# Kernel optimization log

Hardware: AMD Instinct MI355X
Metric: run time of the kernel (lower is better)

The kernel has to match this reference:

```python
import jax, jax.numpy as jnp
import numpy as np


def conv1x1(x, w, b):
    # x: [B,C,H,W], w: [O,C], b: [O]  (1x1 conv == per-pixel matmul)
    return jnp.einsum('oc,bchw->bohw', w, x) + b[None, :, None, None]


def setup_inputs() -> dict:
    key = jax.random.key(0)
    ks = jax.random.split(key, 8)
    B, C, H, W = 8, 256, 64, 64
    heads, points = 8, 4
    x = jax.random.normal(ks[0], (B, C, H, W), dtype=jnp.float32)
    # small offset weights so sampling grids stay mostly in-range (original inits these to 0)
    w_off = jax.random.normal(ks[1], (heads * points * 2, C), dtype=jnp.float32) * 0.01
    b_off = jax.random.normal(ks[2], (heads * points * 2,), dtype=jnp.float32) * 0.05
    w_attn = jax.random.normal(ks[3], (heads * points, C), dtype=jnp.float32) * 0.02
    b_attn = jnp.full((heads * points,), np.log(1.0 / points), dtype=jnp.float32)
    w_val = jax.random.normal(ks[4], (C, C), dtype=jnp.float32) * (1.0 / np.sqrt(C))
    b_val = jnp.zeros((C,), dtype=jnp.float32)
    w_out = jax.random.normal(ks[5], (C, C), dtype=jnp.float32) * (1.0 / np.sqrt(C))
    b_out = jnp.zeros((C,), dtype=jnp.float32)
    return {"x": x, "w_off": w_off, "b_off": b_off, "w_attn": w_attn, "b_attn": b_attn,
            "w_val": w_val, "b_val": b_val, "w_out": w_out, "b_out": b_out,
            "num_heads": heads, "num_points": points}


def _grid_sample_one(v, g):
    # v: [Cph,H,W] value image; g: [P,H,W,2] sampling grid in [-1,1] (x,y), align_corners=True,
    # bilinear, zero padding. Returns [Cph,P,H,W].
    Cph, H, W = v.shape
    ix = (g[..., 0] + 1.0) * 0.5 * (W - 1)  # [P,H,W]
    iy = (g[..., 1] + 1.0) * 0.5 * (H - 1)
    x0 = jnp.floor(ix); y0 = jnp.floor(iy)
    x1 = x0 + 1.0;      y1 = y0 + 1.0
    wx1 = ix - x0; wx0 = 1.0 - wx1
    wy1 = iy - y0; wy0 = 1.0 - wy1

    def corner(yc, xc, w):
        valid = (xc >= 0) & (xc <= W - 1) & (yc >= 0) & (yc <= H - 1)
        yi = jnp.clip(yc, 0, H - 1).astype(jnp.int32)
        xi = jnp.clip(xc, 0, W - 1).astype(jnp.int32)
        vv = v[:, yi, xi]  # [Cph,P,H,W]
        return vv * (w * valid.astype(w.dtype))[None]

    return (corner(y0, x0, wy0 * wx0) + corner(y0, x1, wy0 * wx1)
            + corner(y1, x0, wy1 * wx0) + corner(y1, x1, wy1 * wx1))


def deformable_attention(x, w_off, b_off, w_attn, b_attn, w_val, b_val, w_out, b_out,
                         num_heads, num_points):
    B, C, H, W = x.shape
    hd, P = num_heads, num_points
    cph = C // hd

    value = conv1x1(x, w_val, b_val)                       # [B,C,H,W]
    offsets = conv1x1(x, w_off, b_off)                     # [B,hd*P*2,H,W]
    attn = conv1x1(x, w_attn, b_attn).reshape(B, hd, P, H, W)
    attn = jax.nn.softmax(attn, axis=2)                    # softmax over points

    gy = jnp.linspace(-1.0, 1.0, H, dtype=x.dtype)
    gx = jnp.linspace(-1.0, 1.0, W, dtype=x.dtype)
    base = jnp.stack(jnp.meshgrid(gx, gy, indexing='xy'), axis=-1)  # [H,W,2] (x,y)

    off = offsets.reshape(B, hd, P, 2, H, W).transpose(0, 1, 2, 4, 5, 3)  # [B,hd,P,H,W,2]
    grid = base[None, None, None] + off                                   # [B,hd,P,H,W,2]

    val = value.reshape(B * hd, cph, H, W)
    grid = grid.reshape(B * hd, P, H, W, 2)
    sampled = jax.vmap(_grid_sample_one)(val, grid)        # [B*hd,cph,P,H,W]
    sampled = sampled.reshape(B, hd, cph, P, H, W)

    weighted = (sampled * attn[:, :, None]).sum(axis=3)    # [B,hd,cph,H,W]
    weighted = weighted.reshape(B, C, H, W)
    return conv1x1(weighted, w_out, b_out) + x


def reference(x, w_off, b_off, w_attn, b_attn, w_val, b_val, w_out, b_out,
              num_heads, num_points):
    return deformable_attention(x, w_off, b_off, w_attn, b_attn, w_val, b_val,
                                w_out, b_out, num_heads, num_points)
```

## Files before the change

### kernel.cpp

```cpp
#include <hip/hip_runtime.h>
#include <cstddef>

#define HW 4096

typedef __attribute__((ext_vector_type(8))) short short8v;
typedef __attribute__((ext_vector_type(4))) float f32x4;

__device__ inline unsigned short f2bf(float f) {
    unsigned int u = __float_as_uint(f);
    u += 0x7FFFu + ((u >> 16) & 1u);
    return (unsigned short)(u >> 16);
}
__device__ inline float bf2f(unsigned short s) {
    return __uint_as_float(((unsigned int)s) << 16);
}

__device__ inline void load_tile2(const unsigned short* __restrict__ g, int kc,
                                  int wid, int lane, short8v r[2])
{
    const int s  = lane & 7;
    const int r8 = lane >> 3;
    const unsigned short* src = g + kc + s * 8;
#pragma unroll
    for (int i = 0; i < 2; ++i) {
        const int row = wid * 16 + i * 8 + r8;
        r[i] = *(const short8v*)(src + row * 256);
    }
}

__device__ inline void store_tile2(unsigned short* lds, int wid, int lane, const short8v r[2])
{
    const int s  = lane & 7;
    const int r8 = lane >> 3;
#pragma unroll
    for (int i = 0; i < 2; ++i) {
        const int row = wid * 16 + i * 8 + r8;
        *(short8v*)((char*)lds + row * 128 + ((s ^ (row & 7)) << 4)) = r[i];
    }
}

__device__ inline short8v read_frag(const unsigned short* lds, int row, int kbyte, int lane)
{
    const char* p = (const char*)lds + row * 128 + (kbyte ^ ((lane & 7) * 16));
    return *(const short8v*)p;
}

__global__ __launch_bounds__(256)
void prep_kernel(const float* __restrict__ w_off, const float* __restrict__ b_off,
                 const float* __restrict__ w_attn, const float* __restrict__ b_attn,
                 const float* __restrict__ w_val, const float* __restrict__ b_val,
                 const float* __restrict__ w_out,
                 unsigned short* __restrict__ wcat_bf, unsigned short* __restrict__ wauxlo,
                 unsigned short* __restrict__ wout_bf, float* __restrict__ bcat)
{
    int i = blockIdx.x * 256 + threadIdx.x;
    if (i < 384 * 256) {
        int n = i >> 8, k = i & 255;
        float v;
        if (n < 256)      v = w_val[n * 256 + k];
        else if (n < 320) v = w_off[(n - 256) * 256 + k];
        else if (n < 352) v = w_attn[(n - 320) * 256 + k];
        else              v = 0.0f;
        unsigned short hi = f2bf(v);
        wcat_bf[i] = hi;
        if (n >= 256) wauxlo[(n - 256) * 256 + k] = f2bf(v - bf2f(hi));
    }
    if (i < 128 * 256) {
        int n = i >> 8;
        if (n >= 96) wauxlo[i] = 0;
    }
    if (i < 256 * 256) wout_bf[i] = f2bf(w_out[i]);
    if (i < 512) {
        float v = 0.0f;
        if (i < 256)      v = b_val[i];
        else if (i < 320) v = b_off[i - 256];
        else if (i < 352) v = b_attn[i - 320];
        bcat[i] = v;
    }
}

__global__ __launch_bounds__(256)
void transpose_kernel(const float* __restrict__ x, unsigned short* __restrict__ xhi)
{
    __shared__ float t[64][65];
    const int bid = blockIdx.x;
    const int pt = bid & 63, ct = (bid >> 6) & 3, b = bid >> 8;
    const int tid = threadIdx.x;
    const int rr = tid >> 4, c4 = (tid & 15) * 4;

    const float* src = x + ((size_t)(b * 256 + ct * 64)) * HW + pt * 64;
#pragma unroll
    for (int j = 0; j < 4; ++j) {
        float4 v = *(const float4*)&src[(size_t)(j * 16 + rr) * HW + c4];
        t[j * 16 + rr][c4 + 0] = v.x; t[j * 16 + rr][c4 + 1] = v.y;
        t[j * 16 + rr][c4 + 2] = v.z; t[j * 16 + rr][c4 + 3] = v.w;
    }
    __syncthreads();

    const size_t obase = ((size_t)b * HW + pt * 64) * 256 + ct * 64;
#pragma unroll
    for (int j = 0; j < 4; ++j) {
        int p = j * 16 + rr;
        ushort4 hi = make_ushort4(f2bf(t[c4 + 0][p]), f2bf(t[c4 + 1][p]),
                                  f2bf(t[c4 + 2][p]), f2bf(t[c4 + 3][p]));
        *(ushort4*)&xhi[obase + (size_t)p * 256 + c4] = hi;
    }
}

__device__ inline void mainloop8(const unsigned short* __restrict__ Ag,
                                 const unsigned short* __restrict__ Bg,
                                 unsigned short* Al, unsigned short* Bl,
                                 int wid, int lane, int wm, int wn, f32x4 acc[4][2])
{
    const int mloc = lane & 15, ksel = lane >> 4;
    short8v rA[2], rB[2];
    load_tile2(Ag, 0, wid, lane, rA);
    load_tile2(Bg, 0, wid, lane, rB);
#pragma unroll
    for (int kc = 0; kc < 4; ++kc) {
        if (kc) __syncthreads();
        store_tile2(Al, wid, lane, rA);
        store_tile2(Bl, wid, lane, rB);
        __syncthreads();
        if (kc < 3) {
            load_tile2(Ag, (kc + 1) * 64, wid, lane, rA);
            load_tile2(Bg, (kc + 1) * 64, wid, lane, rB);
        }
#pragma unroll
        for (int kk = 0; kk < 2; ++kk) {
            const int kb = kk * 64 + ksel * 16;
            short8v a[4], bb[2];
#pragma unroll
            for (int f = 0; f < 4; ++f) a[f]  = read_frag(Al, wm * 64 + f * 16 + mloc, kb, lane);
#pragma unroll
            for (int f = 0; f < 2; ++f) bb[f] = read_frag(Bl, wn * 32 + f * 16 + mloc, kb, lane);
#pragma unroll
            for (int fm = 0; fm < 4; ++fm)
#pragma unroll
                for (int fn = 0; fn < 2; ++fn)
                    acc[fm][fn] = __builtin_amdgcn_mfma_f32_16x16x32_bf16(a[fm], bb[fn], acc[fm][fn], 0, 0, 0);
        }
    }
}

__global__ __launch_bounds__(512)
void proj_kernel(const unsigned short* __restrict__ wcat_bf, const unsigned short* __restrict__ wauxlo,
                 const unsigned short* __restrict__ xhi, const float* __restrict__ bcat,
                 unsigned short* __restrict__ value_bf,
                 float* __restrict__ off_ws, float* __restrict__ attn_ws)
{
    __shared__ unsigned short lds[3 * 128 * 64];
    unsigned short* Al  = lds;
    unsigned short* Bl  = lds + 128 * 64;
    unsigned short* Alo = lds + 2 * 128 * 64;

    const int bid = blockIdx.x;
    const int pt = bid & 31;
    const int mt = (bid >> 5) % 3;
    const int b  = bid / 96;
    const int tid = threadIdx.x, wid = tid >> 6, lane = tid & 63;
    const int wm = wid >> 2, wn = wid & 3;
    const int mloc = lane & 15, ksel = lane >> 4;

    const unsigned short* Bg = xhi + ((size_t)b * HW + pt * 128) * 256;

    f32x4 acc[4][2];
#pragma unroll
    for (int fm = 0; fm < 4; ++fm) {
        float4 bv = *(const float4*)&bcat[mt * 128 + wm * 64 + fm * 16 + ksel * 4];
#pragma unroll
        for (int fn = 0; fn < 2; ++fn) acc[fm][fn] = (f32x4){bv.x, bv.y, bv.z, bv.w};
    }

    if (mt < 2) {
        mainloop8(wcat_bf + mt * 128 * 256, Bg, Al, Bl, wid, lane, wm, wn, acc);

#pragma unroll
        for (int fm = 0; fm < 4; ++fm) {
            const int ch = mt * 128 + wm * 64 + fm * 16 + ksel * 4;
            const int head = ch >> 5, c32 = ch & 31;
#pragma unroll
            for (int fn = 0; fn < 2; ++fn) {
                const int p = pt * 128 + wn * 32 + fn * 16 + mloc;
                f32x4 v = acc[fm][fn];
                ushort4 st = make_ushort4(f2bf(v[0]), f2bf(v[1]), f2bf(v[2]), f2bf(v[3]));
                *(ushort4*)&value_bf[(((size_t)(b * 8 + head)) * HW + p) * 32 + c32] = st;
            }
        }
    } else {
        const unsigned short* Ahg = wcat_bf + 256 * 256;
        const unsigned short* Alg = wauxlo;
        short8v rA[2], rL[2], rB[2];
        load_tile2(Ahg, 0, wid, lane, rA);
        load_tile2(Alg, 0, wid, lane, rL);
        load_tile2(Bg, 0, wid, lane, rB);
#pragma unroll
        for (int kc = 0; kc < 4; ++kc) {
            if (kc) __syncthreads();
            store_tile2(Al, wid, lane, rA);
            store_tile2(Alo, wid, lane, rL);
            store_tile2(Bl, wid, lane, rB);
            __syncthreads();
            if (kc < 3) {
                load_tile2(Ahg, (kc + 1) * 64, wid, lane, rA);
                load_tile2(Alg, (kc + 1) * 64, wid, lane, rL);
                load_tile2(Bg, (kc + 1) * 64, wid, lane, rB);
            }
#pragma unroll
            for (int kk = 0; kk < 2; ++kk) {
                const int kb = kk * 64 + ksel * 16;
                short8v ah[4], al[4], bb[2];
#pragma unroll
                for (int f = 0; f < 4; ++f) {
                    ah[f] = read_frag(Al,  wm * 64 + f * 16 + mloc, kb, lane);
                    al[f] = read_frag(Alo, wm * 64 + f * 16 + mloc, kb, lane);
                }
#pragma unroll
                for (int f = 0; f < 2; ++f) bb[f] = read_frag(Bl, wn * 32 + f * 16 + mloc, kb, lane);
#pragma unroll
                for (int fm = 0; fm < 4; ++fm)
#pragma unroll
                    for (int fn = 0; fn < 2; ++fn) {
                        acc[fm][fn] = __builtin_amdgcn_mfma_f32_16x16x32_bf16(ah[fm], bb[fn], acc[fm][fn], 0, 0, 0);
                        acc[fm][fn] = __builtin_amdgcn_mfma_f32_16x16x32_bf16(al[fm], bb[fn], acc[fm][fn], 0, 0, 0);
                    }
            }
        }
#pragma unroll
        for (int fm = 0; fm < 4; ++fm) {
            const int ch0 = wm * 64 + fm * 16 + ksel * 4;
#pragma unroll
            for (int fn = 0; fn < 2; ++fn) {
                const int p = pt * 128 + wn * 32 + fn * 16 + mloc;
                f32x4 v = acc[fm][fn];
                if (ch0 < 64) {
                    *(float4*)&off_ws[((size_t)b * HW + p) * 64 + ch0] =
                        make_float4(v[0], v[1], v[2], v[3]);
                } else if (ch0 < 96) {
                    *(float4*)&attn_ws[((size_t)b * HW + p) * 32 + (ch0 - 64)] =
                        make_float4(v[0], v[1], v[2], v[3]);
                }
            }
        }
    }
}

__global__ __launch_bounds__(256)
void sample_kernel(const unsigned short* __restrict__ value_bf, const float* __restrict__ off_ws,
                   const float* __restrict__ attn_ws, unsigned short* __restrict__ wgt_t)
{
    const int bid    = blockIdx.x;
    const int ptile  = bid & 127;
    const int head   = (bid >> 7) & 7;
    const int b      = bid >> 10;
    const int tid    = threadIdx.x;
    const int c4     = tid & 7;
    const int posIdx = tid >> 3;
    const int p      = ptile * 32 + posIdx;
    const int h      = p >> 6;
    const int w      = p & 63;

    const float gx = w * (2.0f / 63.0f) - 1.0f;
    const float gy = h * (2.0f / 63.0f) - 1.0f;

    float4 la = *(const float4*)&attn_ws[((size_t)b * HW + p) * 32 + head * 4];
    float m  = fmaxf(fmaxf(la.x, la.y), fmaxf(la.z, la.w));
    float e0 = __expf(la.x - m), e1 = __expf(la.y - m), e2 = __expf(la.z - m), e3 = __expf(la.w - m);
    float inv = 1.0f / (e0 + e1 + e2 + e3);
    float aw[4] = {e0 * inv, e1 * inv, e2 * inv, e3 * inv};

    float4 acc = make_float4(0.f, 0.f, 0.f, 0.f);
    const unsigned short* vb = value_bf + (size_t)(b * 8 + head) * HW * 32 + c4 * 4;
    const float* offp = off_ws + ((size_t)b * HW + p) * 64 + head * 8;

#pragma unroll
    for (int pt = 0; pt < 4; ++pt) {
        float ox = offp[pt * 2 + 0];
        float oy = offp[pt * 2 + 1];
        float ix = (gx + ox + 1.0f) * 31.5f;
        float iy = (gy + oy + 1.0f) * 31.5f;
        float x0f = floorf(ix), y0f = floorf(iy);
        float wx1 = ix - x0f, wx0 = 1.0f - wx1;
        float wy1 = iy - y0f, wy0 = 1.0f - wy1;
        int x0 = (int)x0f, y0 = (int)y0f;
        int x1 = x0 + 1,   y1 = y0 + 1;
        float a = aw[pt];
        float vx0 = (x0 >= 0 && x0 <= 63) ? 1.f : 0.f;
        float vx1 = (x1 >= 0 && x1 <= 63) ? 1.f : 0.f;
        float vy0 = (y0 >= 0 && y0 <= 63) ? 1.f : 0.f;
        float vy1 = (y1 >= 0 && y1 <= 63) ? 1.f : 0.f;
        float w00 = a * wy0 * wx0 * vy0 * vx0;
        float w01 = a * wy0 * wx1 * vy0 * vx1;
        float w10 = a * wy1 * wx0 * vy1 * vx0;
        float w11 = a * wy1 * wx1 * vy1 * vx1;
        int cx0 = min(max(x0, 0), 63), cx1 = min(max(x1, 0), 63);
        int cy0 = min(max(y0, 0), 63), cy1 = min(max(y1, 0), 63);
        ushort4 u00 = *(const ushort4*)&vb[(size_t)(cy0 * 64 + cx0) * 32];
        ushort4 u01 = *(const ushort4*)&vb[(size_t)(cy0 * 64 + cx1) * 32];
        ushort4 u10 = *(const ushort4*)&vb[(size_t)(cy1 * 64 + cx0) * 32];
        ushort4 u11 = *(const ushort4*)&vb[(size_t)(cy1 * 64 + cx1) * 32];
        acc.x += w00 * bf2f(u00.x) + w01 * bf2f(u01.x) + w10 * bf2f(u10.x) + w11 * bf2f(u11.x);
        acc.y += w00 * bf2f(u00.y) + w01 * bf2f(u01.y) + w10 * bf2f(u10.y) + w11 * bf2f(u11.y);
        acc.z += w00 * bf2f(u00.z) + w01 * bf2f(u01.z) + w10 * bf2f(u10.z) + w11 * bf2f(u11.z);
        acc.w += w00 * bf2f(u00.w) + w01 * bf2f(u01.w) + w10 * bf2f(u10.w) + w11 * bf2f(u11.w);
    }

    ushort4 st = make_ushort4(f2bf(acc.x), f2bf(acc.y), f2bf(acc.z), f2bf(acc.w));
    *(ushort4*)&wgt_t[((size_t)b * HW + p) * 256 + head * 32 + c4 * 4] = st;
}

__global__ __launch_bounds__(512)
void outproj_gemm(const unsigned short* __restrict__ wout_bf, const unsigned short* __restrict__ wgt_t,
                  const float* __restrict__ b_out, const float* __restrict__ x,
                  float* __restrict__ out)
{
    __shared__ unsigned short Al[128 * 64];
    __shared__ unsigned short Bl[128 * 64];
    const int bid = blockIdx.x;
    const int pt = bid & 31, mt = (bid >> 5) & 1, b = bid >> 6;
    const int tid = threadIdx.x, wid = tid >> 6, lane = tid & 63;
    const int wm = wid >> 2, wn = wid & 3;
    const int mloc = lane & 15, ksel = lane >> 4;

    const unsigned short* Ag = wout_bf + mt * 128 * 256;
    const unsigned short* Bg = wgt_t + ((size_t)b * HW + pt * 128) * 256;

    f32x4 acc[4][2];
#pragma unroll
    for (int fm = 0; fm < 4; ++fm)
#pragma unroll
        for (int fn = 0; fn < 2; ++fn) acc[fm][fn] = (f32x4){0.f, 0.f, 0.f, 0.f};

    mainloop8(Ag, Bg, Al, Bl, wid, lane, wm, wn, acc);

#pragma unroll
    for (int fm = 0; fm < 4; ++fm) {
        const int o = mt * 128 + wm * 64 + fm * 16 + ksel * 4;
        float4 bo = *(const float4*)&b_out[o];
#pragma unroll
        for (int fn = 0; fn < 2; ++fn) {
            const int p = pt * 128 + wn * 32 + fn * 16 + mloc;
            const size_t idx = ((size_t)(b * 256 + o)) * HW + p;
            f32x4 v = acc[fm][fn];
            out[idx + 0 * HW] = v[0] + bo.x + x[idx + 0 * HW];
            out[idx + 1 * HW] = v[1] + bo.y + x[idx + 1 * HW];
            out[idx + 2 * HW] = v[2] + bo.z + x[idx + 2 * HW];
            out[idx + 3 * HW] = v[3] + bo.w + x[idx + 3 * HW];
        }
    }
}

extern "C" void kernel_launch(void* const* d_in, const int* in_sizes, int n_in,
                              void* d_out, int out_size, void* d_ws, size_t ws_size,
                              hipStream_t stream)
{
    const float* x      = (const float*)d_in[0];
    const float* w_off  = (const float*)d_in[1];
    const float* b_off  = (const float*)d_in[2];
    const float* w_attn = (const float*)d_in[3];
    const float* b_attn = (const float*)d_in[4];
    const float* w_val  = (const float*)d_in[5];
    const float* b_val  = (const float*)d_in[6];
    const float* w_out  = (const float*)d_in[7];
    const float* b_out  = (const float*)d_in[8];
    float* out = (float*)d_out;

    char* ws = (char*)d_ws;
    unsigned short* wcat_bf = (unsigned short*)(ws + 0);
    unsigned short* wauxlo  = (unsigned short*)(ws + 196608);
    unsigned short* wout_bf = (unsigned short*)(ws + 262144);
    float*          bcat    = (float*)(ws + 393216);
    unsigned short* xhi     = (unsigned short*)(ws + 395264);
    unsigned short* val_bf  = (unsigned short*)(ws + 17172480);
    float*          off_ws  = (float*)(ws + 33949696);
    float*          attn_ws = (float*)(ws + 42338304);
    unsigned short* wgt_t   = (unsigned short*)(ws + 46532608);

    prep_kernel<<<384, 256, 0, stream>>>(w_off, b_off, w_attn, b_attn, w_val, b_val,
                                         w_out, wcat_bf, wauxlo, wout_bf, bcat);
    transpose_kernel<<<2048, 256, 0, stream>>>(x, xhi);
    proj_kernel<<<768, 512, 0, stream>>>(wcat_bf, wauxlo, xhi, bcat, val_bf, off_ws, attn_ws);
    sample_kernel<<<8192, 256, 0, stream>>>(val_bf, off_ws, attn_ws, wgt_t);
    outproj_gemm<<<512, 512, 0, stream>>>(wout_bf, wgt_t, b_out, x, out);
}
```

Baseline: 76.48 us.

## Fuse bilinear sampling with output projection GEMM via shared memory

Merges the sampling kernel and the output-projection GEMM into one kernel. Each block samples all 8 heads for 64 positions into an XOR-swizzled LDS tile, then multiplies that tile by W_out streamed through LDS. This drops the bf16 round trip of the weighted tensor through global memory and one launch. The point softmax also moves into the projection epilogue. In exchange the grid shrinks to 512 blocks of 512 threads with heavy LDS use. That may lower occupancy and latency hiding for the gather-bound sampling phase, and W_out is reloaded by every block.

Result: faster. 72.14 us (-5.7%).

```diff
diff --git a/kernel.cpp b/kernel.cpp
--- a/kernel.cpp
+++ b/kernel.cpp
@@ -2,6 +2,7 @@
 #include <cstddef>
 
 #define HW 4096
+#define WPITCH 264
 
 typedef __attribute__((ext_vector_type(8))) short short8v;
 typedef __attribute__((ext_vector_type(4))) float f32x4;
@@ -237,111 +238,152 @@
                     *(float4*)&off_ws[((size_t)b * HW + p) * 64 + ch0] =
                         make_float4(v[0], v[1], v[2], v[3]);
                 } else if (ch0 < 96) {
+                    float m  = fmaxf(fmaxf(v[0], v[1]), fmaxf(v[2], v[3]));
+                    float e0 = __expf(v[0] - m), e1 = __expf(v[1] - m);
+                    float e2 = __expf(v[2] - m), e3 = __expf(v[3] - m);
+                    float inv = 1.0f / (e0 + e1 + e2 + e3);
                     *(float4*)&attn_ws[((size_t)b * HW + p) * 32 + (ch0 - 64)] =
-                        make_float4(v[0], v[1], v[2], v[3]);
+                        make_float4(e0 * inv, e1 * inv, e2 * inv, e3 * inv);
                 }
             }
         }
     }
 }
 
-__global__ __launch_bounds__(256)
-void sample_kernel(const unsigned short* __restrict__ value_bf, const float* __restrict__ off_ws,
-                   const float* __restrict__ attn_ws, unsigned short* __restrict__ wgt_t)
-{
-    const int bid    = blockIdx.x;
-    const int ptile  = bid & 127;
-    const int head   = (bid >> 7) & 7;
-    const int b      = bid >> 10;
-    const int tid    = threadIdx.x;
-    const int c4     = tid & 7;
-    const int posIdx = tid >> 3;
-    const int p      = ptile * 32 + posIdx;
-    const int h      = p >> 6;
-    const int w      = p & 63;
-
-    const float gx = w * (2.0f / 63.0f) - 1.0f;
-    const float gy = h * (2.0f / 63.0f) - 1.0f;
-
-    float4 la = *(const float4*)&attn_ws[((size_t)b * HW + p) * 32 + head * 4];
-    float m  = fmaxf(fmaxf(la.x, la.y), fmaxf(la.z, la.w));
-    float e0 = __expf(la.x - m), e1 = __expf(la.y - m), e2 = __expf(la.z - m), e3 = __expf(la.w - m);
-    float inv = 1.0f / (e0 + e1 + e2 + e3);
-    float aw[4] = {e0 * inv, e1 * inv, e2 * inv, e3 * inv};
-
-    float4 acc = make_float4(0.f, 0.f, 0.f, 0.f);
-    const unsigned short* vb = value_bf + (size_t)(b * 8 + head) * HW * 32 + c4 * 4;
-    const float* offp = off_ws + ((size_t)b * HW + p) * 64 + head * 8;
-
-#pragma unroll
-    for (int pt = 0; pt < 4; ++pt) {
-        float ox = offp[pt * 2 + 0];
-        float oy = offp[pt * 2 + 1];
-        float ix = (gx + ox + 1.0f) * 31.5f;
-        float iy = (gy + oy + 1.0f) * 31.5f;
-        float x0f = floorf(ix), y0f = floorf(iy);
-        float wx1 = ix - x0f, wx0 = 1.0f - wx1;
-        float wy1 = iy - y0f, wy0 = 1.0f - wy1;
-        int x0 = (int)x0f, y0 = (int)y0f;
-        int x1 = x0 + 1,   y1 = y0 + 1;
-        float a = aw[pt];
-        float vx0 = (x0 >= 0 && x0 <= 63) ? 1.f : 0.f;
-        float vx1 = (x1 >= 0 && x1 <= 63) ? 1.f : 0.f;
-        float vy0 = (y0 >= 0 && y0 <= 63) ? 1.f : 0.f;
-        float vy1 = (y1 >= 0 && y1 <= 63) ? 1.f : 0.f;
-        float w00 = a * wy0 * wx0 * vy0 * vx0;
-        float w01 = a * wy0 * wx1 * vy0 * vx1;
-        float w10 = a * wy1 * wx0 * vy1 * vx0;
-        float w11 = a * wy1 * wx1 * vy1 * vx1;
-        int cx0 = min(max(x0, 0), 63), cx1 = min(max(x1, 0), 63);
-        int cy0 = min(max(y0, 0), 63), cy1 = min(max(y1, 0), 63);
-        ushort4 u00 = *(const ushort4*)&vb[(size_t)(cy0 * 64 + cx0) * 32];
-        ushort4 u01 = *(const ushort4*)&vb[(size_t)(cy0 * 64 + cx1) * 32];
-        ushort4 u10 = *(const ushort4*)&vb[(size_t)(cy1 * 64 + cx0) * 32];
-        ushort4 u11 = *(const ushort4*)&vb[(size_t)(cy1 * 64 + cx1) * 32];
-        acc.x += w00 * bf2f(u00.x) + w01 * bf2f(u01.x) + w10 * bf2f(u10.x) + w11 * bf2f(u11.x);
-        acc.y += w00 * bf2f(u00.y) + w01 * bf2f(u01.y) + w10 * bf2f(u10.y) + w11 * bf2f(u11.y);
-        acc.z += w00 * bf2f(u00.z) + w01 * bf2f(u01.z) + w10 * bf2f(u10.z) + w11 * bf2f(u11.z);
-        acc.w += w00 * bf2f(u00.w) + w01 * bf2f(u01.w) + w10 * bf2f(u10.w) + w11 * bf2f(u11.w);
-    }
-
-    ushort4 st = make_ushort4(f2bf(acc.x), f2bf(acc.y), f2bf(acc.z), f2bf(acc.w));
-    *(ushort4*)&wgt_t[((size_t)b * HW + p) * 256 + head * 32 + c4 * 4] = st;
-}
-
 __global__ __launch_bounds__(512)
-void outproj_gemm(const unsigned short* __restrict__ wout_bf, const unsigned short* __restrict__ wgt_t,
-                  const float* __restrict__ b_out, const float* __restrict__ x,
-                  float* __restrict__ out)
-{
-    __shared__ unsigned short Al[128 * 64];
-    __shared__ unsigned short Bl[128 * 64];
+void sampleout_kernel(const unsigned short* __restrict__ value_bf,
+                      const float* __restrict__ off_ws, const float* __restrict__ attn_ws,
+                      const unsigned short* __restrict__ wout_bf, const float* __restrict__ b_out,
+                      const float* __restrict__ x, float* __restrict__ out)
+{
+    __shared__ unsigned short Wp[64 * WPITCH];
+    __shared__ unsigned short Asm[256 * 64];
+
     const int bid = blockIdx.x;
-    const int pt = bid & 31, mt = (bid >> 5) & 1, b = bid >> 6;
-    const int tid = threadIdx.x, wid = tid >> 6, lane = tid & 63;
-    const int wm = wid >> 2, wn = wid & 3;
+    const int pt = bid & 63, b = bid >> 6;
+    const int tid = threadIdx.x;
+
+    {
+        const int c4     = tid & 7;
+        const int posIdx = tid >> 3;
+        const int p      = pt * 64 + posIdx;
+        const int h      = p >> 6;
+        const int w      = p & 63;
+        const float gx = w * (2.0f / 63.0f) - 1.0f;
+        const float gy = h * (2.0f / 63.0f) - 1.0f;
+
+        const float* awp  = attn_ws + ((size_t)b * HW + p) * 32;
+        const float* offp = off_ws + ((size_t)b * HW + p) * 64;
+
+#pragma unroll
+        for (int head = 0; head < 8; ++head) {
+            float4 aw4 = *(const float4*)&awp[head * 4];
+            float aw[4] = {aw4.x, aw4.y, aw4.z, aw4.w};
+            float4 o01 = *(const float4*)&offp[head * 8];
+            float4 o23 = *(const float4*)&offp[head * 8 + 4];
+            float oxv[4] = {o01.x, o01.z, o23.x, o23.z};
+            float oyv[4] = {o01.y, o01.w, o23.y, o23.w};
+
+            float4 acc = make_float4(0.f, 0.f, 0.f, 0.f);
+            const unsigned short* vb = value_bf + (size_t)(b * 8 + head) * HW * 32 + c4 * 4;
+#pragma unroll
+            for (int ptq = 0; ptq < 4; ++ptq) {
+                float ix = (gx + oxv[ptq] + 1.0f) * 31.5f;
+                float iy = (gy + oyv[ptq] + 1.0f) * 31.5f;
+                float x0f = floorf(ix), y0f = floorf(iy);
+                float wx1 = ix - x0f, wx0 = 1.0f - wx1;
+                float wy1 = iy - y0f, wy0 = 1.0f - wy1;
+                int x0 = (int)x0f, y0 = (int)y0f;
+                int x1 = x0 + 1,   y1 = y0 + 1;
+                float a = aw[ptq];
+                float vx0 = (x0 >= 0 && x0 <= 63) ? 1.f : 0.f;
+                float vx1 = (x1 >= 0 && x1 <= 63) ? 1.f : 0.f;
+                float vy0 = (y0 >= 0 && y0 <= 63) ? 1.f : 0.f;
+                float vy1 = (y1 >= 0 && y1 <= 63) ? 1.f : 0.f;
+                float w00 = a * wy0 * wx0 * vy0 * vx0;
+                float w01 = a * wy0 * wx1 * vy0 * vx1;
+                float w10 = a * wy1 * wx0 * vy1 * vx0;
+                float w11 = a * wy1 * wx1 * vy1 * vx1;
+                int cx0 = min(max(x0, 0), 63), cx1 = min(max(x1, 0), 63);
+                int cy0 = min(max(y0, 0), 63), cy1 = min(max(y1, 0), 63);
+                ushort4 u00 = *(const ushort4*)&vb[(size_t)(cy0 * 64 + cx0) * 32];
+                ushort4 u01 = *(const ushort4*)&vb[(size_t)(cy0 * 64 + cx1) * 32];
+                ushort4 u10 = *(const ushort4*)&vb[(size_t)(cy1 * 64 + cx0) * 32];
+                ushort4 u11 = *(const ushort4*)&vb[(size_t)(cy1 * 64 + cx1) * 32];
+                acc.x += w00 * bf2f(u00.x) + w01 * bf2f(u01.x) + w10 * bf2f(u10.x) + w11 * bf2f(u11.x);
+                acc.y += w00 * bf2f(u00.y) + w01 * bf2f(u01.y) + w10 * bf2f(u10.y) + w11 * bf2f(u11.y);
+                acc.z += w00 * bf2f(u00.z) + w01 * bf2f(u01.z) + w10 * bf2f(u10.z) + w11 * bf2f(u11.z);
+                acc.w += w00 * bf2f(u00.w) + w01 * bf2f(u01.w) + w10 * bf2f(u10.w) + w11 * bf2f(u11.w);
+            }
+            const int slot = head * 4 + (c4 >> 1);
+            const int byte = posIdx * (WPITCH * 2) + ((slot ^ (posIdx & 7)) << 4) + (c4 & 1) * 8;
+            ushort4 st = make_ushort4(f2bf(acc.x), f2bf(acc.y), f2bf(acc.z), f2bf(acc.w));
+            *(ushort4*)((char*)Wp + byte) = st;
+        }
+    }
+    __syncthreads();
+
+    const int wid = tid >> 6, lane = tid & 63;
+    const int wm = wid & 3, wn = wid >> 2;
     const int mloc = lane & 15, ksel = lane >> 4;
-
-    const unsigned short* Ag = wout_bf + mt * 128 * 256;
-    const unsigned short* Bg = wgt_t + ((size_t)b * HW + pt * 128) * 256;
-
-    f32x4 acc[4][2];
+    const int s = lane & 7, r8 = lane >> 3;
+
+    f32x4 acc2[4][2];
 #pragma unroll
     for (int fm = 0; fm < 4; ++fm)
 #pragma unroll
-        for (int fn = 0; fn < 2; ++fn) acc[fm][fn] = (f32x4){0.f, 0.f, 0.f, 0.f};
-
-    mainloop8(Ag, Bg, Al, Bl, wid, lane, wm, wn, acc);
+        for (int fn = 0; fn < 2; ++fn) acc2[fm][fn] = (f32x4){0.f, 0.f, 0.f, 0.f};
+
+    short8v rA[4];
+#pragma unroll
+    for (int i = 0; i < 4; ++i)
+        rA[i] = *(const short8v*)(wout_bf + (wid * 32 + i * 8 + r8) * 256 + s * 8);
+
+#pragma unroll
+    for (int kc = 0; kc < 4; ++kc) {
+        if (kc) __syncthreads();
+#pragma unroll
+        for (int i = 0; i < 4; ++i) {
+            const int row = wid * 32 + i * 8 + r8;
+            *(short8v*)((char*)Asm + row * 128 + ((s ^ (row & 7)) << 4)) = rA[i];
+        }
+        __syncthreads();
+        if (kc < 3) {
+#pragma unroll
+            for (int i = 0; i < 4; ++i)
+                rA[i] = *(const short8v*)(wout_bf + (wid * 32 + i * 8 + r8) * 256 + (kc + 1) * 64 + s * 8);
+        }
+#pragma unroll
+        for (int kk = 0; kk < 2; ++kk) {
+            short8v a[4], bb[2];
+#pragma unroll
+            for (int f = 0; f < 4; ++f) {
+                const int row = wm * 64 + f * 16 + mloc;
+                a[f] = *(const short8v*)((char*)Asm + row * 128 + (((kk * 4 + ksel) ^ (row & 7)) << 4));
+            }
+#pragma unroll
+            for (int f = 0; f < 2; ++f) {
+                const int row = wn * 32 + f * 16 + mloc;
+                const int slot = kc * 8 + kk * 4 + ksel;
+                bb[f] = *(const short8v*)((char*)Wp + row * (WPITCH * 2) + ((slot ^ (row & 7)) << 4));
+            }
+#pragma unroll
+            for (int fm = 0; fm < 4; ++fm)
+#pragma unroll
+                for (int fn = 0; fn < 2; ++fn)
+                    acc2[fm][fn] = __builtin_amdgcn_mfma_f32_16x16x32_bf16(a[fm], bb[fn], acc2[fm][fn], 0, 0, 0);
+        }
+    }
 
 #pragma unroll
     for (int fm = 0; fm < 4; ++fm) {
-        const int o = mt * 128 + wm * 64 + fm * 16 + ksel * 4;
+        const int o = wm * 64 + fm * 16 + ksel * 4;
         float4 bo = *(const float4*)&b_out[o];
 #pragma unroll
         for (int fn = 0; fn < 2; ++fn) {
-            const int p = pt * 128 + wn * 32 + fn * 16 + mloc;
+            const int p = pt * 64 + wn * 32 + fn * 16 + mloc;
             const size_t idx = ((size_t)(b * 256 + o)) * HW + p;
-            f32x4 v = acc[fm][fn];
+            f32x4 v = acc2[fm][fn];
             out[idx + 0 * HW] = v[0] + bo.x + x[idx + 0 * HW];
             out[idx + 1 * HW] = v[1] + bo.y + x[idx + 1 * HW];
             out[idx + 2 * HW] = v[2] + bo.z + x[idx + 2 * HW];
@@ -374,12 +416,10 @@
     unsigned short* val_bf  = (unsigned short*)(ws + 17172480);
     float*          off_ws  = (float*)(ws + 33949696);
     float*          attn_ws = (float*)(ws + 42338304);
-    unsigned short* wgt_t   = (unsigned short*)(ws + 46532608);
 
     prep_kernel<<<384, 256, 0, stream>>>(w_off, b_off, w_attn, b_attn, w_val, b_val,
                                          w_out, wcat_bf, wauxlo, wout_bf, bcat);
     transpose_kernel<<<2048, 256, 0, stream>>>(x, xhi);
     proj_kernel<<<768, 512, 0, stream>>>(wcat_bf, wauxlo, xhi, bcat, val_bf, off_ws, attn_ws);
-    sample_kernel<<<8192, 256, 0, stream>>>(val_bf, off_ws, attn_ws, wgt_t);
-    outproj_gemm<<<512, 512, 0, stream>>>(wout_bf, wgt_t, b_out, x, out);
-}
+    sampleout_kernel<<<512, 512, 0, stream>>>(val_bf, off_ws, attn_ws, wout_bf, b_out, x, out);
+}
```

## Remap block indices batch-fastest, move softmax into projection epilogue, batch gather loads

Applied to the files above, without the earlier changes.

Reorders block-index decoding in all three kernels so the batch index varies fastest, which changes how work is spread across the XCDs and their L2 caches. The per-head softmax over points now runs once in the projection epilogue, so the sampling kernel reads weights that are already normalized. In the sampling kernel, offsets are read with vector loads, and all 16 corner addresses and weights are computed before any gather is issued, which exposes more memory-level parallelism at the cost of more registers.

New measurement: 72.37 us. -5.4%, faster.

```diff
diff --git a/kernel.cpp b/kernel.cpp
--- a/kernel.cpp
+++ b/kernel.cpp
@@ -155,9 +155,10 @@
     unsigned short* Alo = lds + 2 * 128 * 64;
 
     const int bid = blockIdx.x;
-    const int pt = bid & 31;
-    const int mt = (bid >> 5) % 3;
-    const int b  = bid / 96;
+    const int b    = bid & 7;
+    const int rest = bid >> 3;
+    const int pt = rest & 31;
+    const int mt = rest >> 5;
     const int tid = threadIdx.x, wid = tid >> 6, lane = tid & 63;
     const int wm = wid >> 2, wn = wid & 3;
     const int mloc = lane & 15, ksel = lane >> 4;
@@ -237,8 +238,12 @@
                     *(float4*)&off_ws[((size_t)b * HW + p) * 64 + ch0] =
                         make_float4(v[0], v[1], v[2], v[3]);
                 } else if (ch0 < 96) {
+                    float m  = fmaxf(fmaxf(v[0], v[1]), fmaxf(v[2], v[3]));
+                    float e0 = __expf(v[0] - m), e1 = __expf(v[1] - m);
+                    float e2 = __expf(v[2] - m), e3 = __expf(v[3] - m);
+                    float inv = 1.0f / (e0 + e1 + e2 + e3);
                     *(float4*)&attn_ws[((size_t)b * HW + p) * 32 + (ch0 - 64)] =
-                        make_float4(v[0], v[1], v[2], v[3]);
+                        make_float4(e0 * inv, e1 * inv, e2 * inv, e3 * inv);
                 }
             }
         }
@@ -246,13 +251,14 @@
 }
 
 __global__ __launch_bounds__(256)
-void sample_kernel(const unsigned short* __restrict__ value_bf, const float* __restrict__ off_ws,
-                   const float* __restrict__ attn_ws, unsigned short* __restrict__ wgt_t)
+void sample_kernel(const unsigned short* __restrict__ value_bf,
+                   const float* __restrict__ off_ws, const float* __restrict__ attn_ws,
+                   unsigned short* __restrict__ wgt_t)
 {
     const int bid    = blockIdx.x;
-    const int ptile  = bid & 127;
-    const int head   = (bid >> 7) & 7;
-    const int b      = bid >> 10;
+    const int b      = bid & 7;
+    const int head   = (bid >> 3) & 7;
+    const int ptile  = bid >> 6;
     const int tid    = threadIdx.x;
     const int c4     = tid & 7;
     const int posIdx = tid >> 3;
@@ -263,47 +269,60 @@
     const float gx = w * (2.0f / 63.0f) - 1.0f;
     const float gy = h * (2.0f / 63.0f) - 1.0f;
 
-    float4 la = *(const float4*)&attn_ws[((size_t)b * HW + p) * 32 + head * 4];
-    float m  = fmaxf(fmaxf(la.x, la.y), fmaxf(la.z, la.w));
-    float e0 = __expf(la.x - m), e1 = __expf(la.y - m), e2 = __expf(la.z - m), e3 = __expf(la.w - m);
-    float inv = 1.0f / (e0 + e1 + e2 + e3);
-    float aw[4] = {e0 * inv, e1 * inv, e2 * inv, e3 * inv};
-
-    float4 acc = make_float4(0.f, 0.f, 0.f, 0.f);
+    float4 aw4 = *(const float4*)&attn_ws[((size_t)b * HW + p) * 32 + head * 4];
+    float aw[4] = {aw4.x, aw4.y, aw4.z, aw4.w};
+    const float* offp = off_ws + ((size_t)b * HW + p) * 64 + head * 8;
+    float4 o01 = *(const float4*)&offp[0];
+    float4 o23 = *(const float4*)&offp[4];
+    float oxv[4] = {o01.x, o01.z, o23.x, o23.z};
+    float oyv[4] = {o01.y, o01.w, o23.y, o23.w};
+
     const unsigned short* vb = value_bf + (size_t)(b * 8 + head) * HW * 32 + c4 * 4;
-    const float* offp = off_ws + ((size_t)b * HW + p) * 64 + head * 8;
-
-#pragma unroll
-    for (int pt = 0; pt < 4; ++pt) {
-        float ox = offp[pt * 2 + 0];
-        float oy = offp[pt * 2 + 1];
-        float ix = (gx + ox + 1.0f) * 31.5f;
-        float iy = (gy + oy + 1.0f) * 31.5f;
+
+    int   adr[4][4];
+    float wc[4][4];
+#pragma unroll
+    for (int ptq = 0; ptq < 4; ++ptq) {
+        float ix = (gx + oxv[ptq] + 1.0f) * 31.5f;
+        float iy = (gy + oyv[ptq] + 1.0f) * 31.5f;
         float x0f = floorf(ix), y0f = floorf(iy);
         float wx1 = ix - x0f, wx0 = 1.0f - wx1;
         float wy1 = iy - y0f, wy0 = 1.0f - wy1;
         int x0 = (int)x0f, y0 = (int)y0f;
         int x1 = x0 + 1,   y1 = y0 + 1;
-        float a = aw[pt];
+        float a = aw[ptq];
         float vx0 = (x0 >= 0 && x0 <= 63) ? 1.f : 0.f;
         float vx1 = (x1 >= 0 && x1 <= 63) ? 1.f : 0.f;
         float vy0 = (y0 >= 0 && y0 <= 63) ? 1.f : 0.f;
         float vy1 = (y1 >= 0 && y1 <= 63) ? 1.f : 0.f;
-        float w00 = a * wy0 * wx0 * vy0 * vx0;
-        float w01 = a * wy0 * wx1 * vy0 * vx1;
-        float w10 = a * wy1 * wx0 * vy1 * vx0;
-        float w11 = a * wy1 * wx1 * vy1 * vx1;
+        wc[ptq][0] = a * wy0 * wx0 * vy0 * vx0;
+        wc[ptq][1] = a * wy0 * wx1 * vy0 * vx1;
+        wc[ptq][2] = a * wy1 * wx0 * vy1 * vx0;
+        wc[ptq][3] = a * wy1 * wx1 * vy1 * vx1;
         int cx0 = min(max(x0, 0), 63), cx1 = min(max(x1, 0), 63);
         int cy0 = min(max(y0, 0), 63), cy1 = min(max(y1, 0), 63);
-        ushort4 u00 = *(const ushort4*)&vb[(size_t)(cy0 * 64 + cx0) * 32];
-        ushort4 u01 = *(const ushort4*)&vb[(size_t)(cy0 * 64 + cx1) * 32];
-        ushort4 u10 = *(const ushort4*)&vb[(size_t)(cy1 * 64 + cx0) * 32];
-        ushort4 u11 = *(const ushort4*)&vb[(size_t)(cy1 * 64 + cx1) * 32];
-        acc.x += w00 * bf2f(u00.x) + w01 * bf2f(u01.x) + w10 * bf2f(u10.x) + w11 * bf2f(u11.x);
-        acc.y += w00 * bf2f(u00.y) + w01 * bf2f(u01.y) + w10 * bf2f(u10.y) + w11 * bf2f(u11.y);
-        acc.z += w00 * bf2f(u00.z) + w01 * bf2f(u01.z) + w10 * bf2f(u10.z) + w11 * bf2f(u11.z);
-        acc.w += w00 * bf2f(u00.w) + w01 * bf2f(u01.w) + w10 * bf2f(u10.w) + w11 * bf2f(u11.w);
-    }
+        adr[ptq][0] = (cy0 * 64 + cx0) * 32;
+        adr[ptq][1] = (cy0 * 64 + cx1) * 32;
+        adr[ptq][2] = (cy1 * 64 + cx0) * 32;
+        adr[ptq][3] = (cy1 * 64 + cx1) * 32;
+    }
+    ushort4 u[4][4];
+#pragma unroll
+    for (int ptq = 0; ptq < 4; ++ptq)
+#pragma unroll
+        for (int c = 0; c < 4; ++c)
+            u[ptq][c] = *(const ushort4*)&vb[adr[ptq][c]];
+    float4 acc = make_float4(0.f, 0.f, 0.f, 0.f);
+#pragma unroll
+    for (int ptq = 0; ptq < 4; ++ptq)
+#pragma unroll
+        for (int c = 0; c < 4; ++c) {
+            float wcc = wc[ptq][c];
+            acc.x += wcc * bf2f(u[ptq][c].x);
+            acc.y += wcc * bf2f(u[ptq][c].y);
+            acc.z += wcc * bf2f(u[ptq][c].z);
+            acc.w += wcc * bf2f(u[ptq][c].w);
+        }
 
     ushort4 st = make_ushort4(f2bf(acc.x), f2bf(acc.y), f2bf(acc.z), f2bf(acc.w));
     *(ushort4*)&wgt_t[((size_t)b * HW + p) * 256 + head * 32 + c4 * 4] = st;
@@ -317,7 +336,9 @@
     __shared__ unsigned short Al[128 * 64];
     __shared__ unsigned short Bl[128 * 64];
     const int bid = blockIdx.x;
-    const int pt = bid & 31, mt = (bid >> 5) & 1, b = bid >> 6;
+    const int b  = bid & 7;
+    const int pt = (bid >> 3) & 31;
+    const int mt = bid >> 8;
     const int tid = threadIdx.x, wid = tid >> 6, lane = tid & 63;
     const int wm = wid >> 2, wn = wid & 3;
     const int mloc = lane & 15, ksel = lane >> 4;
```
